# Kernel optimization log

Measured on AMD Instinct MI355X. Metric: run time of the kernel, lower is better.

## Reference

```python
import jax, jax.numpy as jnp
import numpy as np

ALPHA = 0.2  # LeakyReLU negative slope


def setup_inputs() -> dict:
    key = jax.random.key(0)
    ks = jax.random.split(key, 8)
    B, N, C = 65536, 35, 64
    return {
        "x_target": jax.random.normal(ks[0], (B, C), dtype=jnp.float32),
        "x_neigh": jax.random.normal(ks[1], (B, N, C), dtype=jnp.float32),
        "align_w": jax.random.normal(ks[2], (C, C), dtype=jnp.float32) * 0.05,
        "align_b": jax.random.normal(ks[3], (C,), dtype=jnp.float32) * 0.05,
        "attn1_w": jax.random.normal(ks[4], (16, 2 * C), dtype=jnp.float32) * 0.05,
        "attn1_b": jax.random.normal(ks[5], (16,), dtype=jnp.float32) * 0.05,
        "attn2_w": jax.random.normal(ks[6], (1, 16), dtype=jnp.float32) * 0.05,
        "attn2_b": jax.random.normal(ks[7], (1,), dtype=jnp.float32) * 0.05,
    }


def reference(x_target, x_neigh, align_w, align_b, attn1_w, attn1_b, attn2_w, attn2_b):
    B, N, _ = x_neigh.shape
    # align: Linear(c_in -> c_out) applied to both target and neighbors
    t = x_target @ align_w.T + align_b                 # [B, C]
    n = jnp.einsum('bnc,dc->bnd', x_neigh, align_w) + align_b  # [B, N, C]
    # GAT attention: concat(target broadcast, neigh) -> MLP(2C->16->1)
    a_input = jnp.concatenate([jnp.broadcast_to(t[:, None, :], n.shape), n], axis=-1)  # [B, N, 2C]
    h = jax.nn.relu(jnp.einsum('bnk,hk->bnh', a_input, attn1_w) + attn1_b)  # [B, N, 16]
    e = jax.nn.leaky_relu(jnp.einsum('bnh,oh->bno', h, attn2_w) + attn2_b, ALPHA)[..., 0]  # [B, N]
    attention = jax.nn.softmax(e, axis=-1)             # [B, N]
    h_prime = jnp.einsum('bn,bnc->bc', attention, n)   # weighted neighbor sum [B, C]
    return jax.nn.elu(h_prime)  # concat=True path
```

## Files before the change

### kernel.cpp

```cpp
#include <hip/hip_runtime.h>
#include <math.h>


#define ALPHA 0.2f
static constexpr int Bn = 65536;
static constexpr int Nn = 35;
static constexpr int Cn = 64;

#define DPP_XOR1 0xB1
#define DPP_XOR2 0x4E
#define DPP_HMIR 0x141
#define DPP_MIR  0x140

template<int CTRL>
__device__ __forceinline__ float dpp_mov(float x) {
  int r = __builtin_amdgcn_update_dpp(0, __builtin_bit_cast(int, x), CTRL, 0xF, 0xF, true);
  return __builtin_bit_cast(float, r);
}

__device__ __forceinline__ int h_of_m(int m) {
  int b0 = m & 1, b1 = (m >> 1) & 1, b2 = (m >> 2) & 1, b3 = (m >> 3) & 1;
  return (b0 ^ b2) | ((b1 ^ b2) << 1) | ((b0 ^ b3) << 2) | (b3 << 3);
}

__device__ __forceinline__ float reduce_scatter16(const float p[16], int f1, int f2, int f3, int f4) {
  float q[8];
#pragma unroll
  for (int j = 0; j < 8; ++j) {
    float keep = f1 ? p[2*j+1] : p[2*j];
    float send = f1 ? p[2*j]   : p[2*j+1];
    q[j] = keep + dpp_mov<DPP_XOR1>(send);
  }
  float r[4];
#pragma unroll
  for (int j = 0; j < 4; ++j) {
    float keep = f2 ? q[2*j+1] : q[2*j];
    float send = f2 ? q[2*j]   : q[2*j+1];
    r[j] = keep + dpp_mov<DPP_XOR2>(send);
  }
  float s[2];
#pragma unroll
  for (int j = 0; j < 2; ++j) {
    float keep = f3 ? r[2*j+1] : r[2*j];
    float send = f3 ? r[2*j]   : r[2*j+1];
    s[j] = keep + dpp_mov<DPP_HMIR>(send);
  }
  float keep = f4 ? s[1] : s[0];
  float send = f4 ? s[0] : s[1];
  return keep + dpp_mov<DPP_MIR>(send);
}

__device__ __forceinline__ float row_allreduce_add(float x) {
  x += dpp_mov<DPP_XOR1>(x);
  x += dpp_mov<DPP_XOR2>(x);
  x += dpp_mov<DPP_HMIR>(x);
  x += dpp_mov<DPP_MIR>(x);
  return x;
}

__global__ void gat_prep(const float* __restrict__ align_w, const float* __restrict__ align_b,
                         const float* __restrict__ a1w, const float* __restrict__ a1b,
                         float* __restrict__ wsM, float* __restrict__ wsMt, float* __restrict__ wsKt) {
  int t = blockIdx.x * 256 + threadIdx.x;
  if (t < 1024) {
    int h = t >> 6, c = t & 63;
    float accM = 0.f, accMt = 0.f;
    for (int d = 0; d < 64; ++d) {
      float w = align_w[d * 64 + c];
      accM  += a1w[h * 128 + 64 + d] * w;
      accMt += a1w[h * 128 + d] * w;
    }
    wsM[t] = accM;
    wsMt[t] = accMt;
  }
  if (t < 16) {
    float acc = a1b[t];
    for (int d = 0; d < 64; ++d)
      acc += (a1w[t * 128 + d] + a1w[t * 128 + 64 + d]) * align_b[d];
    wsKt[t] = acc;
  }
}

__global__ void gat_u(const float* __restrict__ xt, const float* __restrict__ wsMt,
                      const float* __restrict__ wsKt, float* __restrict__ u_perm) {
  int gt = blockIdx.x * 256 + threadIdx.x;
  int b = gt >> 4, m = gt & 15;
  int hm = h_of_m(m);
  const float4* xr = (const float4*)(xt + (size_t)b * 64);
  const float4* Mr = (const float4*)(wsMt + hm * 64);
  float acc = wsKt[hm];
#pragma unroll
  for (int j = 0; j < 16; ++j) {
    float4 a = Mr[j], x = xr[j];
    acc += a.x * x.x + a.y * x.y + a.z * x.z + a.w * x.w;
  }
  u_perm[gt] = acc;
}

template<bool PRECOMP_U>
__global__ __launch_bounds__(256, 2) void gat_main(
    const float* __restrict__ x_target, const float* __restrict__ x_neigh,
    const float* __restrict__ align_w, const float* __restrict__ align_b,
    const float* __restrict__ attn2_w, const float* __restrict__ attn2_b,
    const float* __restrict__ wsM, const float* __restrict__ wsMt,
    const float* __restrict__ wsKt, const float* __restrict__ u_perm,
    float* __restrict__ out, int waves_total) {
  __shared__ float W_lds[64 * 65];
  __shared__ float xw_lds[4][64];

  int tid = threadIdx.x;
  for (int idx = tid; idx < 4096; idx += 256) {
    int r = idx >> 6, c = idx & 63;
    W_lds[r * 65 + c] = align_w[idx];
  }
  __syncthreads();

  const int lane = tid & 63, wave = tid >> 6;
  const int m = lane & 15, g = lane >> 4;
  const int b0 = m & 1, b1 = (m >> 1) & 1, b2v = (m >> 2) & 1, b3 = (m >> 3) & 1;
  const int f1 = b0 ^ b2v, f2 = b1 ^ b2v, f3 = b0 ^ b3, f4 = b3;
  const int hm = f1 | (f2 << 1) | (f3 << 2) | (f4 << 3);

  float4 Ms[16];
#pragma unroll
  for (int h = 0; h < 16; ++h)
    Ms[h] = ((const float4*)(wsM + h * 64))[m];
  const float w2r = attn2_w[hm];
  const float b2r = attn2_b[0];
  const float biasr = align_b[lane];

  float4 Mts[16];
  float Ktr = 0.f;
  if (!PRECOMP_U) {
#pragma unroll
    for (int h = 0; h < 16; ++h)
      Mts[h] = ((const float4*)(wsMt + h * 64))[m];
    Ktr = wsKt[hm];
  }

  const int gw = blockIdx.x * 4 + wave;
  for (int b = gw; b < Bn; b += waves_total) {
    const float4* xb = (const float4*)(x_neigh + (size_t)b * Nn * Cn);
    float4 x[9];
#pragma unroll
    for (int k = 0; k < 9; ++k) {
      if (k < 8) {
        x[k] = xb[lane + 64 * k];
      } else {
        float4 z; z.x = z.y = z.z = z.w = 0.f;
        if (lane < 48) z = xb[lane + 512];
        x[8] = z;
      }
    }

    float uval;
    if (PRECOMP_U) {
      uval = u_perm[(size_t)b * 16 + m];
    } else {
      float4 xt = ((const float4*)(x_target + (size_t)b * 64))[m];
      float up[16];
#pragma unroll
      for (int h = 0; h < 16; ++h)
        up[h] = Mts[h].x * xt.x + Mts[h].y * xt.y + Mts[h].z * xt.z + Mts[h].w * xt.w;
      uval = reduce_scatter16(up, f1, f2, f3, f4) + Ktr;
    }

    float ex[9];
    float mloc = -1e30f;
#pragma unroll
    for (int k = 0; k < 9; ++k) {
      float p[16];
#pragma unroll
      for (int h = 0; h < 16; ++h)
        p[h] = Ms[h].x * x[k].x + Ms[h].y * x[k].y + Ms[h].z * x[k].z + Ms[h].w * x[k].w;
      float P = reduce_scatter16(p, f1, f2, f3, f4);
      float rr = fmaxf(P + uval, 0.f) * w2r;
      float esum = row_allreduce_add(rr) + b2r;
      float e = fmaxf(esum, 0.f) + ALPHA * fminf(esum, 0.f);
      if (k == 8 && g == 3) e = -1e30f;
      ex[k] = e;
      mloc = fmaxf(mloc, e);
    }

    mloc = fmaxf(mloc, __shfl_xor(mloc, 16));
    mloc = fmaxf(mloc, __shfl_xor(mloc, 32));
    float sloc = 0.f;
#pragma unroll
    for (int k = 0; k < 9; ++k) {
      ex[k] = __expf(ex[k] - mloc);
      sloc += ex[k];
    }
    sloc += __shfl_xor(sloc, 16);
    sloc += __shfl_xor(sloc, 32);
    const float rS = 1.f / sloc;

    float4 xw; xw.x = xw.y = xw.z = xw.w = 0.f;
#pragma unroll
    for (int k = 0; k < 9; ++k) {
      xw.x = fmaf(ex[k], x[k].x, xw.x);
      xw.y = fmaf(ex[k], x[k].y, xw.y);
      xw.z = fmaf(ex[k], x[k].z, xw.z);
      xw.w = fmaf(ex[k], x[k].w, xw.w);
    }
    xw.x += __shfl_xor(xw.x, 16); xw.x += __shfl_xor(xw.x, 32);
    xw.y += __shfl_xor(xw.y, 16); xw.y += __shfl_xor(xw.y, 32);
    xw.z += __shfl_xor(xw.z, 16); xw.z += __shfl_xor(xw.z, 32);
    xw.w += __shfl_xor(xw.w, 16); xw.w += __shfl_xor(xw.w, 32);
    xw.x *= rS; xw.y *= rS; xw.z *= rS; xw.w *= rS;

    if (g == 0)
      *(float4*)(&xw_lds[wave][4 * m]) = xw;
    asm volatile("s_waitcnt lgkmcnt(0)" ::: "memory");

    float hp = biasr;
#pragma unroll
    for (int t = 0; t < 16; ++t) {
      float4 xv = *(const float4*)(&xw_lds[wave][4 * t]);
      hp = fmaf(W_lds[lane * 65 + 4 * t + 0], xv.x, hp);
      hp = fmaf(W_lds[lane * 65 + 4 * t + 1], xv.y, hp);
      hp = fmaf(W_lds[lane * 65 + 4 * t + 2], xv.z, hp);
      hp = fmaf(W_lds[lane * 65 + 4 * t + 3], xv.w, hp);
    }
    float en = __expf(fminf(hp, 0.f)) - 1.f;
    out[(size_t)b * 64 + lane] = hp > 0.f ? hp : en;
  }
}

extern "C" void kernel_launch(void* const* d_in, const int* in_sizes, int n_in,
                              void* d_out, int out_size, void* d_ws, size_t ws_size,
                              hipStream_t stream) {
  const float* x_target = (const float*)d_in[0];
  const float* x_neigh  = (const float*)d_in[1];
  const float* align_w  = (const float*)d_in[2];
  const float* align_b  = (const float*)d_in[3];
  const float* attn1_w  = (const float*)d_in[4];
  const float* attn1_b  = (const float*)d_in[5];
  const float* attn2_w  = (const float*)d_in[6];
  const float* attn2_b  = (const float*)d_in[7];
  float* out = (float*)d_out;

  float* ws = (float*)d_ws;
  float* wsM  = ws;
  float* wsMt = ws + 1024;
  float* wsKt = ws + 2048;
  float* u_perm = ws + 2064;
  size_t need = (2064 + (size_t)Bn * 16) * sizeof(float);
  bool precomp = ws_size >= need;

  gat_prep<<<4, 256, 0, stream>>>(align_w, align_b, attn1_w, attn1_b, wsM, wsMt, wsKt);

  const int blocks = 1024;
  const int waves_total = blocks * 4;
  if (precomp) {
    gat_u<<<(Bn * 16) / 256, 256, 0, stream>>>(x_target, wsMt, wsKt, u_perm);
    gat_main<true><<<blocks, 256, 0, stream>>>(x_target, x_neigh, align_w, align_b,
                                               attn2_w, attn2_b, wsM, wsMt, wsKt,
                                               u_perm, out, waves_total);
  } else {
    gat_main<false><<<blocks, 256, 0, stream>>>(x_target, x_neigh, align_w, align_b,
                                                attn2_w, attn2_b, wsM, wsMt, wsKt,
                                                u_perm, out, waves_total);
  }
}
```

Baseline: 843.6 us.

## Use packed FP32 math, fixed-pattern reduce-scatter, and higher occupancy in GAT kernel

Replaces the lane-dependent keep/send selects in the reduce-scatter with a fixed pattern. Each lane's weight rows are permuted at load time so that the output head equals the lane index m. The per-head dot products and the final 64x64 projection now use inline v_pk_mul_f32/v_pk_fma_f32 packed FP32 instructions. Launch bounds rise to 3 blocks per SIMD and the grid to 2048 blocks, aiming to cut VALU select overhead and hide memory latency better. The trade-off is register pressure under the tighter launch bound (possible spills) and reliance on the permutation being exactly correct.

```diff
diff --git a/kernel.cpp b/kernel.cpp
--- a/kernel.cpp
+++ b/kernel.cpp
@@ -7,6 +7,9 @@
 static constexpr int Nn = 35;
 static constexpr int Cn = 64;
 
+typedef float v2f __attribute__((ext_vector_type(2)));
+typedef float v4f __attribute__((ext_vector_type(4)));
+
 #define DPP_XOR1 0xB1
 #define DPP_XOR2 0x4E
 #define DPP_HMIR 0x141
@@ -18,36 +21,30 @@
   return __builtin_bit_cast(float, r);
 }
 
-__device__ __forceinline__ int h_of_m(int m) {
-  int b0 = m & 1, b1 = (m >> 1) & 1, b2 = (m >> 2) & 1, b3 = (m >> 3) & 1;
-  return (b0 ^ b2) | ((b1 ^ b2) << 1) | ((b0 ^ b3) << 2) | (b3 << 3);
-}
-
-__device__ __forceinline__ float reduce_scatter16(const float p[16], int f1, int f2, int f3, int f4) {
+__device__ __forceinline__ v2f pk_mul(v2f a, v2f b) {
+  v2f d; asm("v_pk_mul_f32 %0, %1, %2" : "=v"(d) : "v"(a), "v"(b)); return d;
+}
+__device__ __forceinline__ v2f pk_fma(v2f a, v2f b, v2f c) {
+  v2f d; asm("v_pk_fma_f32 %0, %1, %2, %3" : "=v"(d) : "v"(a), "v"(b), "v"(c)); return d;
+}
+
+__device__ __forceinline__ int perm_h(int pos, int m) {
+  int p3 = (pos >> 3) & 1;
+  int e  = ((pos >> 2) ^ (pos >> 3)) & 1;
+  return (pos ^ m) ^ (e ? 3 : 0) ^ (p3 ? 4 : 0);
+}
+
+__device__ __forceinline__ float reduce_scatter16(const float p[16]) {
   float q[8];
 #pragma unroll
-  for (int j = 0; j < 8; ++j) {
-    float keep = f1 ? p[2*j+1] : p[2*j];
-    float send = f1 ? p[2*j]   : p[2*j+1];
-    q[j] = keep + dpp_mov<DPP_XOR1>(send);
-  }
+  for (int j = 0; j < 8; ++j) q[j] = p[2*j] + dpp_mov<DPP_XOR1>(p[2*j+1]);
   float r[4];
 #pragma unroll
-  for (int j = 0; j < 4; ++j) {
-    float keep = f2 ? q[2*j+1] : q[2*j];
-    float send = f2 ? q[2*j]   : q[2*j+1];
-    r[j] = keep + dpp_mov<DPP_XOR2>(send);
-  }
+  for (int j = 0; j < 4; ++j) r[j] = q[2*j] + dpp_mov<DPP_XOR2>(q[2*j+1]);
   float s[2];
 #pragma unroll
-  for (int j = 0; j < 2; ++j) {
-    float keep = f3 ? r[2*j+1] : r[2*j];
-    float send = f3 ? r[2*j]   : r[2*j+1];
-    s[j] = keep + dpp_mov<DPP_HMIR>(send);
-  }
-  float keep = f4 ? s[1] : s[0];
-  float send = f4 ? s[0] : s[1];
-  return keep + dpp_mov<DPP_MIR>(send);
+  for (int j = 0; j < 2; ++j) s[j] = r[2*j] + dpp_mov<DPP_HMIR>(r[2*j+1]);
+  return s[0] + dpp_mov<DPP_MIR>(s[1]);
 }
 
 __device__ __forceinline__ float row_allreduce_add(float x) {
@@ -82,28 +79,27 @@
 }
 
 __global__ void gat_u(const float* __restrict__ xt, const float* __restrict__ wsMt,
-                      const float* __restrict__ wsKt, float* __restrict__ u_perm) {
+                      const float* __restrict__ wsKt, float* __restrict__ u_arr) {
   int gt = blockIdx.x * 256 + threadIdx.x;
-  int b = gt >> 4, m = gt & 15;
-  int hm = h_of_m(m);
-  const float4* xr = (const float4*)(xt + (size_t)b * 64);
-  const float4* Mr = (const float4*)(wsMt + hm * 64);
-  float acc = wsKt[hm];
+  int b = gt >> 4, h = gt & 15;
+  const v4f* xr = (const v4f*)(xt + (size_t)b * 64);
+  const v4f* Mr = (const v4f*)(wsMt + h * 64);
+  float acc = wsKt[h];
 #pragma unroll
   for (int j = 0; j < 16; ++j) {
-    float4 a = Mr[j], x = xr[j];
+    v4f a = Mr[j], x = xr[j];
     acc += a.x * x.x + a.y * x.y + a.z * x.z + a.w * x.w;
   }
-  u_perm[gt] = acc;
-}
-
-template<bool PRECOMP_U>
-__global__ __launch_bounds__(256, 2) void gat_main(
+  u_arr[gt] = acc;
+}
+
+template<bool PRECOMP_U, int MINWAVES>
+__global__ __launch_bounds__(256, MINWAVES) void gat_main(
     const float* __restrict__ x_target, const float* __restrict__ x_neigh,
     const float* __restrict__ align_w, const float* __restrict__ align_b,
     const float* __restrict__ attn2_w, const float* __restrict__ attn2_b,
     const float* __restrict__ wsM, const float* __restrict__ wsMt,
-    const float* __restrict__ wsKt, const float* __restrict__ u_perm,
+    const float* __restrict__ wsKt, const float* __restrict__ u_arr,
     float* __restrict__ out, int waves_total) {
   __shared__ float W_lds[64 * 65];
   __shared__ float xw_lds[4][64];
@@ -117,63 +113,76 @@
 
   const int lane = tid & 63, wave = tid >> 6;
   const int m = lane & 15, g = lane >> 4;
-  const int b0 = m & 1, b1 = (m >> 1) & 1, b2v = (m >> 2) & 1, b3 = (m >> 3) & 1;
-  const int f1 = b0 ^ b2v, f2 = b1 ^ b2v, f3 = b0 ^ b3, f4 = b3;
-  const int hm = f1 | (f2 << 1) | (f3 << 2) | (f4 << 3);
-
-  float4 Ms[16];
-#pragma unroll
-  for (int h = 0; h < 16; ++h)
-    Ms[h] = ((const float4*)(wsM + h * 64))[m];
-  const float w2r = attn2_w[hm];
+
+  v2f Mlo[16], Mhi[16];
+#pragma unroll
+  for (int pos = 0; pos < 16; ++pos) {
+    int h = perm_h(pos, m);
+    v4f Mv = ((const v4f*)(wsM + h * 64))[m];
+    Mlo[pos] = __builtin_shufflevector(Mv, Mv, 0, 1);
+    Mhi[pos] = __builtin_shufflevector(Mv, Mv, 2, 3);
+  }
+  const float w2r = attn2_w[m];
   const float b2r = attn2_b[0];
   const float biasr = align_b[lane];
-
-  float4 Mts[16];
+  const int wrow = lane * 65;
+
+  v2f Mtlo[16], Mthi[16];
   float Ktr = 0.f;
   if (!PRECOMP_U) {
 #pragma unroll
-    for (int h = 0; h < 16; ++h)
-      Mts[h] = ((const float4*)(wsMt + h * 64))[m];
-    Ktr = wsKt[hm];
+    for (int pos = 0; pos < 16; ++pos) {
+      int h = perm_h(pos, m);
+      v4f Mv = ((const v4f*)(wsMt + h * 64))[m];
+      Mtlo[pos] = __builtin_shufflevector(Mv, Mv, 0, 1);
+      Mthi[pos] = __builtin_shufflevector(Mv, Mv, 2, 3);
+    }
+    Ktr = wsKt[m];
   }
 
   const int gw = blockIdx.x * 4 + wave;
   for (int b = gw; b < Bn; b += waves_total) {
-    const float4* xb = (const float4*)(x_neigh + (size_t)b * Nn * Cn);
-    float4 x[9];
-#pragma unroll
-    for (int k = 0; k < 9; ++k) {
-      if (k < 8) {
-        x[k] = xb[lane + 64 * k];
-      } else {
-        float4 z; z.x = z.y = z.z = z.w = 0.f;
-        if (lane < 48) z = xb[lane + 512];
-        x[8] = z;
-      }
+    const v4f* xb = (const v4f*)(x_neigh + (size_t)b * Nn * Cn);
+    v4f x[9];
+#pragma unroll
+    for (int k = 0; k < 8; ++k) x[k] = xb[lane + 64 * k];
+    {
+      v4f z = {0.f, 0.f, 0.f, 0.f};
+      if (lane < 48) z = xb[512 + lane];
+      x[8] = z;
     }
 
     float uval;
     if (PRECOMP_U) {
-      uval = u_perm[(size_t)b * 16 + m];
+      uval = u_arr[(size_t)b * 16 + m];
     } else {
-      float4 xt = ((const float4*)(x_target + (size_t)b * 64))[m];
+      v4f xt4 = ((const v4f*)(x_target + (size_t)b * 64))[m];
+      v2f xtlo = __builtin_shufflevector(xt4, xt4, 0, 1);
+      v2f xthi = __builtin_shufflevector(xt4, xt4, 2, 3);
       float up[16];
 #pragma unroll
-      for (int h = 0; h < 16; ++h)
-        up[h] = Mts[h].x * xt.x + Mts[h].y * xt.y + Mts[h].z * xt.z + Mts[h].w * xt.w;
-      uval = reduce_scatter16(up, f1, f2, f3, f4) + Ktr;
+      for (int pos = 0; pos < 16; ++pos) {
+        v2f t = pk_mul(Mtlo[pos], xtlo);
+        t = pk_fma(Mthi[pos], xthi, t);
+        up[pos] = t.x + t.y;
+      }
+      uval = reduce_scatter16(up) + Ktr;
     }
 
     float ex[9];
     float mloc = -1e30f;
 #pragma unroll
     for (int k = 0; k < 9; ++k) {
+      v2f xlo = __builtin_shufflevector(x[k], x[k], 0, 1);
+      v2f xhi = __builtin_shufflevector(x[k], x[k], 2, 3);
       float p[16];
 #pragma unroll
-      for (int h = 0; h < 16; ++h)
-        p[h] = Ms[h].x * x[k].x + Ms[h].y * x[k].y + Ms[h].z * x[k].z + Ms[h].w * x[k].w;
-      float P = reduce_scatter16(p, f1, f2, f3, f4);
+      for (int pos = 0; pos < 16; ++pos) {
+        v2f t = pk_mul(Mlo[pos], xlo);
+        t = pk_fma(Mhi[pos], xhi, t);
+        p[pos] = t.x + t.y;
+      }
+      float P = reduce_scatter16(p);
       float rr = fmaxf(P + uval, 0.f) * w2r;
       float esum = row_allreduce_add(rr) + b2r;
       float e = fmaxf(esum, 0.f) + ALPHA * fminf(esum, 0.f);
@@ -194,7 +203,7 @@
     sloc += __shfl_xor(sloc, 32);
     const float rS = 1.f / sloc;
 
-    float4 xw; xw.x = xw.y = xw.z = xw.w = 0.f;
+    v4f xw = {0.f, 0.f, 0.f, 0.f};
 #pragma unroll
     for (int k = 0; k < 9; ++k) {
       xw.x = fmaf(ex[k], x[k].x, xw.x);
@@ -206,21 +215,24 @@
     xw.y += __shfl_xor(xw.y, 16); xw.y += __shfl_xor(xw.y, 32);
     xw.z += __shfl_xor(xw.z, 16); xw.z += __shfl_xor(xw.z, 32);
     xw.w += __shfl_xor(xw.w, 16); xw.w += __shfl_xor(xw.w, 32);
-    xw.x *= rS; xw.y *= rS; xw.z *= rS; xw.w *= rS;
+    xw *= rS;
 
     if (g == 0)
-      *(float4*)(&xw_lds[wave][4 * m]) = xw;
+      *(v4f*)(&xw_lds[wave][4 * m]) = xw;
     asm volatile("s_waitcnt lgkmcnt(0)" ::: "memory");
 
-    float hp = biasr;
+    v2f hp2 = {0.f, 0.f};
 #pragma unroll
     for (int t = 0; t < 16; ++t) {
-      float4 xv = *(const float4*)(&xw_lds[wave][4 * t]);
-      hp = fmaf(W_lds[lane * 65 + 4 * t + 0], xv.x, hp);
-      hp = fmaf(W_lds[lane * 65 + 4 * t + 1], xv.y, hp);
-      hp = fmaf(W_lds[lane * 65 + 4 * t + 2], xv.z, hp);
-      hp = fmaf(W_lds[lane * 65 + 4 * t + 3], xv.w, hp);
-    }
+      v2f xv0 = *(const v2f*)(&xw_lds[wave][4 * t]);
+      v2f xv1 = *(const v2f*)(&xw_lds[wave][4 * t + 2]);
+      int a = wrow + 4 * t;
+      v2f w0 = { W_lds[a],     W_lds[a + 1] };
+      v2f w1 = { W_lds[a + 2], W_lds[a + 3] };
+      hp2 = pk_fma(w0, xv0, hp2);
+      hp2 = pk_fma(w1, xv1, hp2);
+    }
+    float hp = biasr + hp2.x + hp2.y;
     float en = __expf(fminf(hp, 0.f)) - 1.f;
     out[(size_t)b * 64 + lane] = hp > 0.f ? hp : en;
   }
@@ -243,22 +255,22 @@
   float* wsM  = ws;
   float* wsMt = ws + 1024;
   float* wsKt = ws + 2048;
-  float* u_perm = ws + 2064;
+  float* u_arr = ws + 2064;
   size_t need = (2064 + (size_t)Bn * 16) * sizeof(float);
   bool precomp = ws_size >= need;
 
   gat_prep<<<4, 256, 0, stream>>>(align_w, align_b, attn1_w, attn1_b, wsM, wsMt, wsKt);
 
-  const int blocks = 1024;
+  const int blocks = 2048;
   const int waves_total = blocks * 4;
   if (precomp) {
-    gat_u<<<(Bn * 16) / 256, 256, 0, stream>>>(x_target, wsMt, wsKt, u_perm);
-    gat_main<true><<<blocks, 256, 0, stream>>>(x_target, x_neigh, align_w, align_b,
-                                               attn2_w, attn2_b, wsM, wsMt, wsKt,
-                                               u_perm, out, waves_total);
+    gat_u<<<(Bn * 16) / 256, 256, 0, stream>>>(x_target, wsMt, wsKt, u_arr);
+    gat_main<true, 3><<<blocks, 256, 0, stream>>>(x_target, x_neigh, align_w, align_b,
+                                                  attn2_w, attn2_b, wsM, wsMt, wsKt,
+                                                  u_arr, out, waves_total);
   } else {
-    gat_main<false><<<blocks, 256, 0, stream>>>(x_target, x_neigh, align_w, align_b,
-                                                attn2_w, attn2_b, wsM, wsMt, wsKt,
-                                                u_perm, out, waves_total);
-  }
-}
+    gat_main<false, 2><<<blocks, 256, 0, stream>>>(x_target, x_neigh, align_w, align_b,
+                                                   attn2_w, attn2_b, wsM, wsMt, wsKt,
+                                                   u_arr, out, waves_total);
+  }
+}
```

New measurement: 821.8 us. -2.6%, faster.
